# Kernel optimization log

Measured on AMD Instinct MI355X. Metric: run time of the kernel, lower is better.

Reference implementation:

```python
import jax, jax.numpy as jnp
import numpy as np

NEG_BIG = 1e9  # large-negative bias used by the original TF code


def setup_inputs() -> dict:
    key = jax.random.key(0)
    kq, kk, kv = jax.random.split(key, 3)
    B, H, W, C, CV = 8, 64, 64, 128, 128
    return {
        "query": jax.random.normal(kq, (B, H, W, C), dtype=jnp.float32),
        "key": jax.random.normal(kk, (B, H, W, C), dtype=jnp.float32),
        "value": jax.random.normal(kv, (B, H, W, CV), dtype=jnp.float32),
    }


def reference(query, key, value):
    B, Hh, Ww, C = query.shape
    CV = value.shape[-1]
    Nq = Hh * Ww                      # canvas_size_q (flattened spatial)
    Nk = key.shape[1] * key.shape[2]  # canvas_size
    q = query.reshape(B, Nq, C)
    k = key.reshape(B, Nk, C)
    v = value.reshape(B, Nk, CV)
    # dense QK^T scores over the flattened canvas: [B, Nq, Nk]
    dot = jnp.einsum('bqc,bkc->bqk', q, k) / jnp.sqrt(jnp.asarray(C, dtype=q.dtype))
    # causal mask: 1 where key position j <= query position i (allowed)
    allowed = jnp.tril(jnp.ones((Nq, Nk), dtype=q.dtype))
    # softmax with large-negative bias on disallowed positions, then re-mask
    probs = jax.nn.softmax(dot - NEG_BIG * (1.0 - allowed), axis=-1) * allowed
    mixed = jnp.einsum('bqk,bkc->bqc', probs, v)
    return mixed.reshape(B, Hh, Ww, CV)
```

## Files before the change

### kernel.cpp

```cpp
#include <hip/hip_runtime.h>
#include <hip/hip_bf16.h>

typedef __bf16 bf16_t;
typedef __attribute__((ext_vector_type(8))) __bf16 bf16x8;
typedef __attribute__((ext_vector_type(4))) __bf16 bf16x4;
typedef __attribute__((ext_vector_type(4))) float floatx4;

static constexpr int NSEQ = 4096;
static constexpr int DIM  = 128;
static constexpr int BATCH = 8;
static constexpr size_t NELEM = (size_t)BATCH * NSEQ * DIM;
static constexpr size_t WS_NEED = 2 * NELEM * sizeof(bf16_t);

static constexpr int NSLOT = 160;
static constexpr size_t WS_SPLITK =
    WS_NEED + (size_t)BATCH * NSLOT * (8192 + 64) * sizeof(float);

static constexpr float SCALE_LOG2E = 0.08838834764831845f * 1.4426950408889634f;

__device__ __forceinline__ int slot_base(int qt) {
  int g = qt >> 4, r = qt & 15;
  return qt + 8 * g * (g - 1) + r * g;
}

__device__ __forceinline__ void gld16(bf16_t* l, const bf16_t* g) {
  __builtin_amdgcn_global_load_lds(
      (const __attribute__((address_space(1))) unsigned int*)g,
      (__attribute__((address_space(3))) unsigned int*)l, 16, 0, 0);
}

__device__ __forceinline__ bf16x8 ld8_f32s(const float* p, float s) {
  float4 a = *(const float4*)p;
  float4 b = *(const float4*)(p + 4);
  bf16x8 r = {(__bf16)(a.x * s), (__bf16)(a.y * s), (__bf16)(a.z * s), (__bf16)(a.w * s),
              (__bf16)(b.x * s), (__bf16)(b.y * s), (__bf16)(b.z * s), (__bf16)(b.w * s)};
  return r;
}


__global__ __launch_bounds__(256)
void prep_kernel(const float* __restrict__ K, const float* __restrict__ V,
                 bf16_t* __restrict__ Kb, bf16_t* __restrict__ Vt) {
  __shared__ bf16_t ldsT[128 * 66];
  const int bid = blockIdx.x;
  if (bid < 1536) {
    const size_t n4 = NELEM / 4;
    for (size_t i = (size_t)bid * 256 + threadIdx.x; i < n4; i += (size_t)1536 * 256) {
      float4 k = ((const float4*)K)[i];
      bf16x4 kv = {(__bf16)k.x, (__bf16)k.y, (__bf16)k.z, (__bf16)k.w};
      ((bf16x4*)Kb)[i] = kv;
    }
  } else {
    const int id = bid - 1536;
    const int b  = id & 7;
    const int kt = id >> 3;
    const float* src = V + ((size_t)(b * NSEQ + kt * 64)) * DIM;
    #pragma unroll
    for (int it = 0; it < 8; ++it) {
      const int idx = it * 256 + (int)threadIdx.x;
      const int k = idx >> 5, c4 = idx & 31;
      float4 v = ((const float4*)src)[idx];
      ldsT[(c4 * 4 + 0) * 66 + k] = (__bf16)v.x;
      ldsT[(c4 * 4 + 1) * 66 + k] = (__bf16)v.y;
      ldsT[(c4 * 4 + 2) * 66 + k] = (__bf16)v.z;
      ldsT[(c4 * 4 + 3) * 66 + k] = (__bf16)v.w;
    }
    __syncthreads();
    #pragma unroll
    for (int it = 0; it < 4; ++it) {
      const int task = it * 256 + (int)threadIdx.x;
      const int d = task >> 3, kg = task & 7;
      bf16x8 o;
      #pragma unroll
      for (int j = 0; j < 8; ++j) o[j] = ldsT[d * 66 + kg * 8 + j];
      *(bf16x8*)(Vt + ((size_t)b * DIM + d) * NSEQ + kt * 64 + kg * 8) = o;
    }
  }
}


template <bool MASK>
__device__ __forceinline__ void tile16(
    const bf16_t* __restrict__ kbuf, const bf16_t* __restrict__ vbuf,
    const bf16x8 (&qf)[4], int l16, int quad, int wq16,
    floatx4 (&acc)[8], float& lsum) {
  #pragma unroll
  for (int h = 0; h < 2; ++h) {
    float pr[8];
    #pragma unroll
    for (int cc = 0; cc < 2; ++cc) {
      const int c4 = 2 * h + cc;
      floatx4 sv = {0.f, 0.f, 0.f, 0.f};
      const bf16_t* krow = kbuf + (c4 * 16 + l16) * DIM;
      #pragma unroll
      for (int d = 0; d < 4; ++d) {
        bf16x8 kf = *(const bf16x8*)(krow + (((4 * d + quad) ^ l16) * 8));
        sv = __builtin_amdgcn_mfma_f32_16x16x32_bf16(kf, qf[d], sv, 0, 0, 0);
      }
      #pragma unroll
      for (int r = 0; r < 4; ++r) {
        float v = sv[r];
        if constexpr (MASK) {
          const int key = 32 * h + 8 * quad + 4 * cc + r;
          v = (key <= wq16 + l16) ? v : -3.0e38f;
        }
        float p = __builtin_amdgcn_exp2f(v);
        lsum += p;
        pr[4 * cc + r] = p;
      }
    }
    bf16x8 pf;
    #pragma unroll
    for (int j = 0; j < 8; ++j) pf[j] = (__bf16)pr[j];
    __builtin_amdgcn_s_setprio(1);
    #pragma unroll
    for (int c = 0; c < 8; ++c) {
      const bf16_t* vrow = vbuf + (c * 16 + l16) * 64;
      bf16x8 vf = *(const bf16x8*)(vrow + (((quad + 4 * h) ^ (l16 & 7)) * 8));
      acc[c] = __builtin_amdgcn_mfma_f32_16x16x32_bf16(pf, vf, acc[c], 0, 0, 0);
    }
    __builtin_amdgcn_s_setprio(0);
  }
}


__global__ __launch_bounds__(256, 3)
void causal_attn_splitk(const float* __restrict__ Qf, const bf16_t* __restrict__ Kb,
                        const bf16_t* __restrict__ Vt, float* __restrict__ Out,
                        float* __restrict__ Pp, float* __restrict__ Ls) {
  __shared__ __align__(16) bf16_t Kds[2][64 * DIM];
  __shared__ __align__(16) bf16_t Vds[DIM * 64];

  const int b = (int)blockIdx.x & 7;
  const int s = (NSLOT - 1) - ((int)blockIdx.x >> 3);
  int qt = 63, cch = 0;
  {
    int acc0 = 0;
    #pragma unroll
    for (int g = 0; g < 4; ++g) {
      const int bandw = 16 * (g + 1);
      if (s < acc0 + bandw) {
        const int u = s - acc0;
        qt = g * 16 + u / (g + 1);
        cch = u % (g + 1);
        break;
      }
      acc0 += bandw;
    }
  }
  const int ntot = qt + 1;
  const int nch  = (qt >> 4) + 1;
  const int nt_c = (ntot - 1 - cch) / nch + 1;
  const int nmask = (cch + (nt_c - 1) * nch == qt) ? 1 : 0;
  const int nfull = nt_c - nmask;

  const int tid  = (int)threadIdx.x;
  const int wave = tid >> 6;
  const int lane = tid & 63;
  const int l16  = lane & 15;
  const int quad = lane >> 4;
  const int wq16 = wave * 16;

  bf16x8 qf[4];
  {
    const float* qrow =
        Qf + ((size_t)b * NSEQ + qt * 64 + wq16 + l16) * DIM + quad * 8;
    #pragma unroll
    for (int d = 0; d < 4; ++d) qf[d] = ld8_f32s(qrow + 32 * d, SCALE_LOG2E);
  }

  const bf16_t* kg = Kb + (size_t)b * NSEQ * DIM;
  const bf16_t* vg = Vt + ((size_t)b * DIM + 32 * wave) * NSEQ;
  int koff[4], voff[4];
  #pragma unroll
  for (int i = 0; i < 4; ++i) {
    const int p    = 16 * wave + 4 * i + quad;
    const int srow = 32 * (wave >> 1) + 8 * i + 4 * (wave & 1) + quad;
    koff[i] = srow * DIM + ((l16 ^ (p & 15)) * 8);
    const int vrow = 8 * i + (lane >> 3);
    voff[i] = vrow * NSEQ + (((lane & 7) ^ (vrow & 7)) * 8);
  }

  floatx4 acc[8];
  #pragma unroll
  for (int c = 0; c < 8; ++c) acc[c] = (floatx4){0.f, 0.f, 0.f, 0.f};
  float lsum = 0.f;

  {
    const size_t kb0 = (size_t)cch * 64;
    bf16_t* kl = &Kds[0][wave * 2048];
    bf16_t* vl = &Vds[wave * 2048];
    #pragma unroll
    for (int i = 0; i < 4; ++i) {
      gld16(kl + i * 512, kg + kb0 * DIM + koff[i]);
      gld16(vl + i * 512, vg + kb0 + voff[i]);
    }
  }
  __syncthreads();

  int t = cch;
  for (int it = 0; it < nt_c; ++it, t += nch) {
    const int cur = it & 1;
    const bool more = (it + 1 < nt_c);
    const size_t kbn = (size_t)(t + nch) * 64;
    if (more) {
      bf16_t* kl = &Kds[cur ^ 1][wave * 2048];
      #pragma unroll
      for (int i = 0; i < 4; ++i) gld16(kl + i * 512, kg + kbn * DIM + koff[i]);
    }
    __builtin_amdgcn_sched_barrier(0);
    if (it < nfull)
      tile16<false>(Kds[cur], Vds, qf, l16, quad, wq16, acc, lsum);
    else
      tile16<true>(Kds[cur], Vds, qf, l16, quad, wq16, acc, lsum);
    __builtin_amdgcn_sched_barrier(0);
    __builtin_amdgcn_s_barrier();
    if (more) {
      bf16_t* vl = &Vds[wave * 2048];
      #pragma unroll
      for (int i = 0; i < 4; ++i) gld16(vl + i * 512, vg + kbn + voff[i]);
      asm volatile("s_waitcnt vmcnt(0)" ::: "memory");
      __builtin_amdgcn_sched_barrier(0);
      __builtin_amdgcn_s_barrier();
    }
  }

  float lred = lsum;
  lred += __shfl_xor(lred, 16, 64);
  lred += __shfl_xor(lred, 32, 64);

  if (nch == 1) {
    float invl[4];
    #pragma unroll
    for (int r = 0; r < 4; ++r)
      invl[r] = 1.0f / __shfl(lred, quad * 4 + r, 64);
    float* orow =
        Out + ((size_t)b * NSEQ + qt * 64 + wq16 + quad * 4) * DIM + l16;
    #pragma unroll
    for (int c = 0; c < 8; ++c)
      #pragma unroll
      for (int r = 0; r < 4; ++r)
        orow[(size_t)r * DIM + c * 16] = acc[c][r] * invl[r];
  } else {
    const int slot = b * NSLOT + slot_base(qt) + cch;
    float* pb = Pp + (size_t)slot * 8192 +
                ((size_t)(wq16 + quad * 4)) * 128 + l16;
    #pragma unroll
    for (int c = 0; c < 8; ++c)
      #pragma unroll
      for (int r = 0; r < 4; ++r)
        pb[(size_t)r * 128 + c * 16] = acc[c][r];
    if (quad == 0)
      Ls[(size_t)slot * 64 + wq16 + l16] = lred;
  }
}


__global__ __launch_bounds__(256)
void combine_kernel(const float* __restrict__ Pp, const float* __restrict__ Ls,
                    float* __restrict__ Out) {
  const int e    = (int)blockIdx.x >> 1;
  const int half = (int)blockIdx.x & 1;
  const int b    = e & 7;
  const int qt   = 16 + (e >> 3);
  const int s0   = b * NSLOT + slot_base(qt);
  const int nch  = (qt >> 4) + 1;
  const int t = (int)threadIdx.x;
  #pragma unroll
  for (int j = 0; j < 4; ++j) {
    const int idx = j * 256 + t;
    const int q   = half * 32 + (idx >> 5);
    const int d4  = idx & 31;
    float4 v = {0.f, 0.f, 0.f, 0.f};
    float  l = 0.f;
    for (int ch = 0; ch < nch; ++ch) {
      const float* pc = Pp + (size_t)(s0 + ch) * 8192 + (size_t)q * 128 + d4 * 4;
      float4 a = *(const float4*)pc;
      v.x += a.x; v.y += a.y; v.z += a.z; v.w += a.w;
      l += Ls[(size_t)(s0 + ch) * 64 + q];
    }
    const float inv = 1.0f / l;
    float4 r = {v.x * inv, v.y * inv, v.z * inv, v.w * inv};
    *(float4*)(Out + ((size_t)b * NSEQ + qt * 64 + q) * DIM + d4 * 4) = r;
  }
}


template <bool MASK>
__device__ __forceinline__ void tile_compute(
    const bf16_t* __restrict__ kbuf, const bf16_t* __restrict__ vbuf,
    bf16_t* __restrict__ pl, const bf16x8 (&qf)[4],
    int l16, int quad, int wq, floatx4 (&acc)[8], float (&lsum)[4]) {
  floatx4 s[4];
  #pragma unroll
  for (int c4 = 0; c4 < 4; ++c4) s[c4] = (floatx4){0.f, 0.f, 0.f, 0.f};
  #pragma unroll
  for (int c4 = 0; c4 < 4; ++c4) {
    const bf16_t* krow = kbuf + (c4 * 16 + l16) * DIM;
    #pragma unroll
    for (int d = 0; d < 4; ++d) {
      bf16x8 kf = *(const bf16x8*)(krow + (((4 * d + quad) ^ l16) * 8));
      s[c4] = __builtin_amdgcn_mfma_f32_16x16x32_bf16(qf[d], kf, s[c4], 0, 0, 0);
    }
  }
  #pragma unroll
  for (int c4 = 0; c4 < 4; ++c4) {
    #pragma unroll
    for (int r = 0; r < 4; ++r) {
      float v = s[c4][r];
      if constexpr (MASK)
        v = (c4 * 16 + l16 <= wq + quad * 4 + r) ? v : -3.0e38f;
      float p = __builtin_amdgcn_exp2f(v);
      lsum[r] += p;
      pl[(quad * 4 + r) * 72 + c4 * 16 + l16] = (__bf16)p;
    }
  }
  asm volatile("s_waitcnt lgkmcnt(0)" ::: "memory");
  bf16x8 pfA = *(const bf16x8*)(pl + l16 * 72 + quad * 8);
  bf16x8 pfB = *(const bf16x8*)(pl + l16 * 72 + 32 + quad * 8);
  #pragma unroll
  for (int c = 0; c < 8; ++c) {
    const bf16_t* vrow = vbuf + (c * 16 + l16) * 64;
    bf16x8 vfA = *(const bf16x8*)(vrow + ((quad ^ (l16 & 7)) * 8));
    bf16x8 vfB = *(const bf16x8*)(vrow + (((quad + 4) ^ (l16 & 7)) * 8));
    acc[c] = __builtin_amdgcn_mfma_f32_16x16x32_bf16(pfA, vfA, acc[c], 0, 0, 0);
    acc[c] = __builtin_amdgcn_mfma_f32_16x16x32_bf16(pfB, vfB, acc[c], 0, 0, 0);
  }
}

__global__ __launch_bounds__(256)
void causal_attn_kernel(const float* __restrict__ Qf, const bf16_t* __restrict__ Kb,
                        const bf16_t* __restrict__ Vt, float* __restrict__ Out) {
  __shared__ __align__(16) bf16_t Kbuf[64 * DIM];
  __shared__ __align__(16) bf16_t Vbuf[DIM * 64];
  __shared__ __align__(16) bf16_t Pbuf[4][16 * 72];

  const int half = blockIdx.x >> 8;
  const int idx  = blockIdx.x & 255;
  const int b    = idx & 7;
  const int q32  = idx >> 3;
  const int qt64 = half ? q32 : 63 - q32;

  const int tid  = (int)threadIdx.x;
  const int wave = tid >> 6;
  const int lane = tid & 63;
  const int l16  = lane & 15;
  const int quad = lane >> 4;
  const int wq   = wave * 16;

  bf16x8 qf[4];
  {
    const float* qrow = Qf + ((size_t)b * NSEQ + qt64 * 64 + wq + l16) * DIM + quad * 8;
    #pragma unroll
    for (int d = 0; d < 4; ++d) qf[d] = ld8_f32s(qrow + 32 * d, SCALE_LOG2E);
  }

  const bf16_t* kg0 = Kb + ((size_t)b * NSEQ + 16 * wave) * DIM;
  const bf16_t* vg0 = Vt + ((size_t)b * DIM + 32 * wave) * NSEQ;
  int koff[4], voff[4];
  #pragma unroll
  for (int i = 0; i < 4; ++i) {
    const int krow = 4 * i + (lane >> 4);
    koff[i] = krow * DIM + (((lane & 15) ^ (krow & 15)) * 8);
    const int vrow = 8 * i + (lane >> 3);
    voff[i] = vrow * NSEQ + (((lane & 7) ^ ((lane >> 3) & 7)) * 8);
  }
  bf16_t* kl = Kbuf + 16 * wave * DIM;
  bf16_t* vl = Vbuf + 32 * wave * 64;
  bf16_t* pl = Pbuf[wave];

  floatx4 acc[8];
  #pragma unroll
  for (int c = 0; c < 8; ++c) acc[c] = (floatx4){0.f, 0.f, 0.f, 0.f};
  float lsum[4] = {0.f, 0.f, 0.f, 0.f};

  const int nk = qt64 + 1;
  for (int kt = 0; kt < nk - 1; ++kt) {
    const int kb = kt * 64;
    #pragma unroll
    for (int i = 0; i < 4; ++i) gld16(kl + i * 512, kg0 + (size_t)kb * DIM + koff[i]);
    #pragma unroll
    for (int i = 0; i < 4; ++i) gld16(vl + i * 512, vg0 + kb + voff[i]);
    __syncthreads();
    tile_compute<false>(Kbuf, Vbuf, pl, qf, l16, quad, wq, acc, lsum);
    __syncthreads();
  }
  {
    const int kb = (nk - 1) * 64;
    #pragma unroll
    for (int i = 0; i < 4; ++i) gld16(kl + i * 512, kg0 + (size_t)kb * DIM + koff[i]);
    #pragma unroll
    for (int i = 0; i < 4; ++i) gld16(vl + i * 512, vg0 + kb + voff[i]);
    __syncthreads();
    tile_compute<true>(Kbuf, Vbuf, pl, qf, l16, quad, wq, acc, lsum);
  }

  float inv_l[4];
  #pragma unroll
  for (int r = 0; r < 4; ++r) {
    float s = lsum[r];
    #pragma unroll
    for (int off = 1; off < 16; off <<= 1) s += __shfl_xor(s, off, 64);
    inv_l[r] = 1.0f / s;
  }
  float* orow = Out + ((size_t)b * NSEQ + qt64 * 64 + wq + quad * 4) * DIM + l16;
  #pragma unroll
  for (int c = 0; c < 8; ++c) {
    #pragma unroll
    for (int r = 0; r < 4; ++r)
      orow[(size_t)r * DIM + c * 16] = acc[c][r] * inv_l[r];
  }
}


__global__ __launch_bounds__(256)
void causal_attn_fb(const float* __restrict__ Qf, const float* __restrict__ Kf,
                    const float* __restrict__ Vf, float* __restrict__ Out) {
  __shared__ bf16_t p_lds[4][16 * 72];
  const int bid = blockIdx.x, t = bid >> 3, b = bid & 7;
  const int tid = (int)threadIdx.x, wave = tid >> 6, lane = tid & 63;
  const int l16 = lane & 15, quad = lane >> 4;
  const int qtile = (wave < 2) ? t : (127 - t);
  const int q_base = qtile * 32 + (wave & 1) * 16;

  bf16x8 qf[4];
  const float* qrow = Qf + ((size_t)b * NSEQ + q_base + l16) * DIM + quad * 8;
  #pragma unroll
  for (int d = 0; d < 4; ++d) qf[d] = ld8_f32s(qrow + 32 * d, SCALE_LOG2E);

  floatx4 acc[8];
  #pragma unroll
  for (int c = 0; c < 8; ++c) acc[c] = (floatx4){0.f, 0.f, 0.f, 0.f};
  float lsum[4] = {0.f, 0.f, 0.f, 0.f};
  bf16_t* pl = p_lds[wave];
  const int ntiles = (q_base + 16 + 63) >> 6;

  for (int kt = 0; kt < ntiles; ++kt) {
    const int kb = kt * 64;
    floatx4 s[4];
    #pragma unroll
    for (int c4 = 0; c4 < 4; ++c4) s[c4] = (floatx4){0.f, 0.f, 0.f, 0.f};
    const float* kbase = Kf + ((size_t)b * NSEQ + kb + l16) * DIM + quad * 8;
    #pragma unroll
    for (int c4 = 0; c4 < 4; ++c4) {
      #pragma unroll
      for (int d = 0; d < 4; ++d) {
        bf16x8 kf = ld8_f32s(kbase + (size_t)c4 * 16 * DIM + 32 * d, 1.0f);
        s[c4] = __builtin_amdgcn_mfma_f32_16x16x32_bf16(qf[d], kf, s[c4], 0, 0, 0);
      }
    }
    #pragma unroll
    for (int c4 = 0; c4 < 4; ++c4) {
      #pragma unroll
      for (int r = 0; r < 4; ++r) {
        float v = s[c4][r];
        const int qi = q_base + quad * 4 + r;
        v = (kb + c4 * 16 + l16 <= qi) ? v : -3.0e38f;
        float p = __builtin_amdgcn_exp2f(v);
        lsum[r] += p;
        pl[(quad * 4 + r) * 72 + c4 * 16 + l16] = (__bf16)p;
      }
    }
    asm volatile("s_waitcnt lgkmcnt(0)" ::: "memory");
    bf16x8 pfA = *(const bf16x8*)(pl + l16 * 72 + quad * 8);
    bf16x8 pfB = *(const bf16x8*)(pl + l16 * 72 + 32 + quad * 8);
    const float* vb = Vf + ((size_t)b * NSEQ + kb) * DIM;
    #pragma unroll
    for (int c = 0; c < 8; ++c) {
      bf16x8 vfA, vfB;
      #pragma unroll
      for (int j = 0; j < 8; ++j) {
        vfA[j] = (__bf16)vb[(size_t)(quad * 8 + j) * DIM + c * 16 + l16];
        vfB[j] = (__bf16)vb[(size_t)(32 + quad * 8 + j) * DIM + c * 16 + l16];
      }
      acc[c] = __builtin_amdgcn_mfma_f32_16x16x32_bf16(pfA, vfA, acc[c], 0, 0, 0);
      acc[c] = __builtin_amdgcn_mfma_f32_16x16x32_bf16(pfB, vfB, acc[c], 0, 0, 0);
    }
  }
  float inv_l[4];
  #pragma unroll
  for (int r = 0; r < 4; ++r) {
    float s = lsum[r];
    #pragma unroll
    for (int off = 1; off < 16; off <<= 1) s += __shfl_xor(s, off, 64);
    inv_l[r] = 1.0f / s;
  }
  float* orow = Out + ((size_t)b * NSEQ + q_base + quad * 4) * DIM + l16;
  #pragma unroll
  for (int c = 0; c < 8; ++c) {
    #pragma unroll
    for (int r = 0; r < 4; ++r)
      orow[(size_t)r * DIM + c * 16] = acc[c][r] * inv_l[r];
  }
}

extern "C" void kernel_launch(void* const* d_in, const int* in_sizes, int n_in,
                              void* d_out, int out_size, void* d_ws, size_t ws_size,
                              hipStream_t stream) {
  const float* Q = (const float*)d_in[0];
  const float* K = (const float*)d_in[1];
  const float* V = (const float*)d_in[2];
  float* Out = (float*)d_out;
  (void)in_sizes; (void)n_in; (void)out_size;

  dim3 block(256);
  if (ws_size >= WS_SPLITK) {
    bf16_t* Kb = (bf16_t*)d_ws;
    bf16_t* Vt = Kb + NELEM;
    float*  Pp = (float*)((char*)d_ws + WS_NEED);
    float*  Ls = Pp + (size_t)BATCH * NSLOT * 8192;
    prep_kernel<<<dim3(2048), block, 0, stream>>>(K, V, Kb, Vt);
    causal_attn_splitk<<<dim3(BATCH * NSLOT), block, 0, stream>>>(Q, Kb, Vt, Out, Pp, Ls);
    combine_kernel<<<dim3(BATCH * 48 * 2), block, 0, stream>>>(Pp, Ls, Out);
  } else if (ws_size >= WS_NEED) {
    bf16_t* Kb = (bf16_t*)d_ws;
    bf16_t* Vt = Kb + NELEM;
    prep_kernel<<<dim3(2048), block, 0, stream>>>(K, V, Kb, Vt);
    causal_attn_kernel<<<dim3(512), block, 0, stream>>>(Q, Kb, Vt, Out);
  } else {
    causal_attn_fb<<<dim3(512), block, 0, stream>>>(Q, K, V, Out);
  }
}
```

Baseline: 154.8 us.

## Read V fragments directly from global memory instead of staging through LDS

Removes the shared-memory V tile and its per-iteration global-to-LDS copy and second barrier. Each wave now loads its PV operand fragments straight from the transposed V buffer in global memory inside the tile loop. This cuts LDS footprint (possibly allowing more occupancy) and one barrier per iteration, but every wave issues redundant global/L2 loads of the same V tile, and the exposed load latency now sits right before the MFMAs instead of being prefetched.

```diff
diff --git a/kernel.cpp b/kernel.cpp
--- a/kernel.cpp
+++ b/kernel.cpp
@@ -80,8 +80,8 @@
 
 
 template <bool MASK>
-__device__ __forceinline__ void tile16(
-    const bf16_t* __restrict__ kbuf, const bf16_t* __restrict__ vbuf,
+__device__ __forceinline__ void tile16v(
+    const bf16_t* __restrict__ kbuf, const bf16_t* __restrict__ vq,
     const bf16x8 (&qf)[4], int l16, int quad, int wq16,
     floatx4 (&acc)[8], float& lsum) {
   #pragma unroll
@@ -115,8 +115,7 @@
     __builtin_amdgcn_s_setprio(1);
     #pragma unroll
     for (int c = 0; c < 8; ++c) {
-      const bf16_t* vrow = vbuf + (c * 16 + l16) * 64;
-      bf16x8 vf = *(const bf16x8*)(vrow + (((quad + 4 * h) ^ (l16 & 7)) * 8));
+      bf16x8 vf = *(const bf16x8*)(vq + (size_t)c * 16 * NSEQ + 32 * h);
       acc[c] = __builtin_amdgcn_mfma_f32_16x16x32_bf16(pf, vf, acc[c], 0, 0, 0);
     }
     __builtin_amdgcn_s_setprio(0);
@@ -129,7 +128,6 @@
                         const bf16_t* __restrict__ Vt, float* __restrict__ Out,
                         float* __restrict__ Pp, float* __restrict__ Ls) {
   __shared__ __align__(16) bf16_t Kds[2][64 * DIM];
-  __shared__ __align__(16) bf16_t Vds[DIM * 64];
 
   const int b = (int)blockIdx.x & 7;
   const int s = (NSLOT - 1) - ((int)blockIdx.x >> 3);
@@ -170,16 +168,14 @@
   }
 
   const bf16_t* kg = Kb + (size_t)b * NSEQ * DIM;
-  const bf16_t* vg = Vt + ((size_t)b * DIM + 32 * wave) * NSEQ;
-  int koff[4], voff[4];
+  int koff[4];
   #pragma unroll
   for (int i = 0; i < 4; ++i) {
     const int p    = 16 * wave + 4 * i + quad;
     const int srow = 32 * (wave >> 1) + 8 * i + 4 * (wave & 1) + quad;
     koff[i] = srow * DIM + ((l16 ^ (p & 15)) * 8);
-    const int vrow = 8 * i + (lane >> 3);
-    voff[i] = vrow * NSEQ + (((lane & 7) ^ (vrow & 7)) * 8);
-  }
+  }
+  const bf16_t* vq0 = Vt + ((size_t)b * DIM + l16) * NSEQ + 8 * quad;
 
   floatx4 acc[8];
   #pragma unroll
@@ -189,12 +185,8 @@
   {
     const size_t kb0 = (size_t)cch * 64;
     bf16_t* kl = &Kds[0][wave * 2048];
-    bf16_t* vl = &Vds[wave * 2048];
-    #pragma unroll
-    for (int i = 0; i < 4; ++i) {
-      gld16(kl + i * 512, kg + kb0 * DIM + koff[i]);
-      gld16(vl + i * 512, vg + kb0 + voff[i]);
-    }
+    #pragma unroll
+    for (int i = 0; i < 4; ++i) gld16(kl + i * 512, kg + kb0 * DIM + koff[i]);
   }
   __syncthreads();
 
@@ -202,27 +194,21 @@
   for (int it = 0; it < nt_c; ++it, t += nch) {
     const int cur = it & 1;
     const bool more = (it + 1 < nt_c);
-    const size_t kbn = (size_t)(t + nch) * 64;
     if (more) {
+      const size_t kbn = (size_t)(t + nch) * 64;
       bf16_t* kl = &Kds[cur ^ 1][wave * 2048];
       #pragma unroll
       for (int i = 0; i < 4; ++i) gld16(kl + i * 512, kg + kbn * DIM + koff[i]);
     }
     __builtin_amdgcn_sched_barrier(0);
+    const bf16_t* vq = vq0 + (size_t)t * 64;
     if (it < nfull)
-      tile16<false>(Kds[cur], Vds, qf, l16, quad, wq16, acc, lsum);
+      tile16v<false>(Kds[cur], vq, qf, l16, quad, wq16, acc, lsum);
     else
-      tile16<true>(Kds[cur], Vds, qf, l16, quad, wq16, acc, lsum);
+      tile16v<true>(Kds[cur], vq, qf, l16, quad, wq16, acc, lsum);
     __builtin_amdgcn_sched_barrier(0);
+    asm volatile("s_waitcnt vmcnt(0)" ::: "memory");
     __builtin_amdgcn_s_barrier();
-    if (more) {
-      bf16_t* vl = &Vds[wave * 2048];
-      #pragma unroll
-      for (int i = 0; i < 4; ++i) gld16(vl + i * 512, vg + kbn + voff[i]);
-      asm volatile("s_waitcnt vmcnt(0)" ::: "memory");
-      __builtin_amdgcn_sched_barrier(0);
-      __builtin_amdgcn_s_barrier();
-    }
   }
 
   float lred = lsum;
```

New measurement: 260.6 us. 68.4% more time.
